# Performance work log

Hardware: AMD Instinct MI355X
Metric: run time of the kernel (lower is better)

The kernel has to match this reference:

```python
import jax, jax.numpy as jnp
import numpy as np

VOCAB, EMB, HID, LAYERS = 23, 16, 256, 8


def _lstm_layer(xseq, Wih, Whh, bih, bhh):
    # xseq: [B,T,D_in]; Wih: [4H,D_in]; Whh: [4H,H]; biases: [4H]
    B = xseq.shape[0]
    H = Whh.shape[1]
    # precompute input contribution to gates for all timesteps
    xg = jnp.einsum('btd,gd->btg', xseq, Wih) + bih + bhh  # [B,T,4H]
    xg = jnp.swapaxes(xg, 0, 1)  # [T,B,4H] for scan

    def step(carry, g_in):
        h, c = carry
        g = g_in + h @ Whh.T  # [B,4H]
        i, f, gg, o = jnp.split(g, 4, axis=-1)  # PyTorch gate order i,f,g,o
        i = jax.nn.sigmoid(i)
        f = jax.nn.sigmoid(f)
        gg = jnp.tanh(gg)
        o = jax.nn.sigmoid(o)
        c = f * c + i * gg
        h = o * jnp.tanh(c)
        return (h, c), h

    h0 = jnp.zeros((B, H), xseq.dtype)
    c0 = jnp.zeros((B, H), xseq.dtype)
    (_, _), hs = jax.lax.scan(step, (h0, c0), xg)
    return jnp.swapaxes(hs, 0, 1)  # [B,T,H]


def setup_inputs() -> dict:
    key = jax.random.key(0)
    ks = jax.random.split(key, 8)
    B, T = 64, 512
    s_e = 1.0 / np.sqrt(HID)
    x = jax.random.randint(ks[0], (B, T), 0, VOCAB)
    emb = jax.random.normal(ks[1], (VOCAB, EMB), jnp.float32)
    W_ih0 = jax.random.uniform(ks[2], (4 * HID, EMB), jnp.float32, -s_e, s_e)
    W_ih_rest = jax.random.uniform(ks[3], (LAYERS - 1, 4 * HID, HID), jnp.float32, -s_e, s_e)
    W_hh = jax.random.uniform(ks[4], (LAYERS, 4 * HID, HID), jnp.float32, -s_e, s_e)
    b_ih = jax.random.uniform(ks[5], (LAYERS, 4 * HID), jnp.float32, -s_e, s_e)
    b_hh = jax.random.uniform(ks[6], (LAYERS, 4 * HID), jnp.float32, -s_e, s_e)
    fc_w = jax.random.uniform(ks[7], (VOCAB, HID), jnp.float32, -s_e, s_e)
    fc_b = jnp.zeros((VOCAB,), jnp.float32)
    return {"x": x, "emb": emb, "W_ih0": W_ih0, "W_ih_rest": W_ih_rest,
            "W_hh": W_hh, "b_ih": b_ih, "b_hh": b_hh, "fc_w": fc_w, "fc_b": fc_b}


def reference(x, emb, W_ih0, W_ih_rest, W_hh, b_ih, b_hh, fc_w, fc_b):
    h = emb[x]  # [B,T,EMB]
    h = _lstm_layer(h, W_ih0, W_hh[0], b_ih[0], b_hh[0])
    for l in range(1, LAYERS):
        h = _lstm_layer(h, W_ih_rest[l - 1], W_hh[l], b_ih[l], b_hh[l])
    return h @ fc_w.T + fc_b  # [B,T,VOCAB]
```

## Files before the change

kernel.cpp:

```cpp
#include <hip/hip_runtime.h>
#include <cstdint>
#include <cstddef>

#define BB   64
#define TT   512
#define HH   256
#define G4   1024
#define NL   8
#define NW   32
#define HPW  8
#define NR   32

#define POLL_BOUND (1 << 15)

typedef _Float16 half8 __attribute__((ext_vector_type(8)));
typedef float   floatx4 __attribute__((ext_vector_type(4)));

__device__ __forceinline__ float sigm(float v)   { return 1.0f / (1.0f + __expf(-v)); }
__device__ __forceinline__ float tanh_f(float v) { return 1.0f - 2.0f / (__expf(2.0f * v) + 1.0f); }

__device__ __forceinline__ void gstore8_x(_Float16* p, half8 d) {
  asm volatile("global_store_dwordx4 %0, %1, off sc0 sc1" :: "v"(p), "v"(d) : "memory");
}
__device__ __forceinline__ void stdword_x(int* p, int v) {
  asm volatile("global_store_dword %0, %1, off sc0 sc1" :: "v"(p), "v"(v) : "memory");
}
__device__ __forceinline__ void wait_vm0() {
  asm volatile("s_waitcnt vmcnt(0)" ::: "memory");
}
__device__ __forceinline__ int ldflag_x(const int* p) {
  int v; asm volatile("global_load_dword %0, %1, off sc0 sc1" : "=v"(v) : "v"(p) : "memory");
  wait_vm0(); return v;
}

#define TSTRIDE ((size_t)32 * BB * 8)
#define LSTRIDE ((size_t)TT * TSTRIDE)

__global__ void build_xg0(const float* __restrict__ emb, const float* __restrict__ Wih0,
                          float* __restrict__ table) {
  int i = blockIdx.x * 256 + threadIdx.x;
  if (i >= 23 * G4) return;
  int v = i >> 10, n = i & (G4 - 1);
  float a = 0.f;
#pragma unroll
  for (int e = 0; e < 16; ++e) a += emb[v * 16 + e] * Wih0[n * 16 + e];
  table[i] = a;
}

__global__ __launch_bounds__(256, 1) void lstm_pipeline(
    const int*   __restrict__ x,
    const float* __restrict__ Wih_rest,
    const float* __restrict__ Whh,
    const float* __restrict__ bih,
    const float* __restrict__ bhh,
    const float* __restrict__ xg0t,
    _Float16* __restrict__ hseq,
    int* __restrict__ cnt)
{
  const int l   = blockIdx.x & 7;
  const int w   = blockIdx.x >> 3;
  const int tid = threadIdx.x;
  const int lane = tid & 63;
  const int p    = tid >> 6;

  __shared__ __align__(16) _Float16 wlds[64 * NR * 8];
  __shared__ __align__(16) _Float16 hl[BB * 8];
  __shared__ float  blds[NR];
  __shared__ float  tlds[23 * NR];

  for (int idx = tid; idx < 64 * NR; idx += 256) {
    int kc = idx >> 5;
    int n  = idx & 31;
    int g = n >> 3, jl = n & 7;
    int gr = g * 256 + w * HPW + jl;
    float v[8];
    if (kc < 32) {
      if (l == 0) { for (int j = 0; j < 8; ++j) v[j] = 0.f; }
      else {
        const float* src = Wih_rest + ((size_t)(l - 1) * G4 + gr) * HH + kc * 8;
        for (int j = 0; j < 8; ++j) v[j] = src[j];
      }
    } else {
      const float* src = Whh + ((size_t)l * G4 + gr) * HH + (kc - 32) * 8;
      for (int j = 0; j < 8; ++j) v[j] = src[j];
    }
    _Float16* dst = wlds + (size_t)idx * 8;
    for (int j = 0; j < 8; ++j) dst[j] = (_Float16)v[j];
  }
  if (tid < NR) {
    int g = tid >> 3, jl = tid & 7;
    int gr = g * 256 + w * HPW + jl;
    blds[tid] = bih[l * G4 + gr] + bhh[l * G4 + gr];
  }
  if (l == 0) {
    for (int idx = tid; idx < 23 * NR; idx += 256) {
      int v = idx >> 5, n = idx & 31;
      int g = n >> 3, jl = n & 7;
      tlds[idx] = xg0t[v * G4 + g * 256 + w * HPW + jl];
    }
  }
  if (tid == 0) (void)__hip_atomic_load(cnt, __ATOMIC_ACQUIRE, __HIP_MEMORY_SCOPE_AGENT);
  __syncthreads();

  const int arow = p * 16 + (lane & 15);
  const int kq   = lane >> 4;
  const int n0   = lane & 15;
  const int n1   = 16 + n0;
  const int cu   = lane & 7;
  const bool lowh = (n0 < 8);
  const int roff = lowh ? 0 : 2;
  const int rowb = p * 16 + kq * 4;

  const _Float16* hin  = hseq + (size_t)(l > 0 ? l - 1 : 0) * LSTRIDE;
  _Float16*       hrec = hseq + (size_t)l * LSTRIDE;

  const float bi = blds[cu], bf = blds[8 + cu], bg = blds[16 + cu], bo = blds[24 + cu];

  float cst[2] = {0.f, 0.f};

  for (int t = 0; t < TT; ++t) {
    floatx4 acc0 = {0.f, 0.f, 0.f, 0.f};
    floatx4 acc1 = {0.f, 0.f, 0.f, 0.f};

    if (l > 0 && t > 0) {
      const _Float16* ain = hin + (size_t)t * TSTRIDE;
      half8 aA[8];
#pragma unroll
      for (int kt = 0; kt < 8; ++kt) {
        int kc = kt * 4 + kq;
        aA[kt] = *(const half8*)(ain + ((size_t)(kc * 64 + arow) << 3));
      }
#pragma unroll
      for (int kt = 0; kt < 8; ++kt) {
        int kc = kt * 4 + kq;
        half8 w0 = *(const half8*)(wlds + ((kc * 32 + n0) << 3));
        half8 w1 = *(const half8*)(wlds + ((kc * 32 + n1) << 3));
        acc0 = __builtin_amdgcn_mfma_f32_16x16x32_f16(aA[kt], w0, acc0, 0, 0, 0);
        acc1 = __builtin_amdgcn_mfma_f32_16x16x32_f16(aA[kt], w1, acc1, 0, 0, 0);
      }
    }

    if (t > 0 && p == 3) {
      const int* f = cnt + l * NW;
      for (int it = 0; it < POLL_BOUND; ++it) {
        int v = ldflag_x(f + (lane & 31));
        if (__all(v >= t)) break;
        __builtin_amdgcn_s_sleep(1);
      }
    }
    if (l > 0 && p == 2) {
      const int tgt = (t + 2 < TT) ? t + 2 : TT;
      const int* f = cnt + (l - 1) * NW;
      for (int it = 0; it < POLL_BOUND; ++it) {
        int v = ldflag_x(f + (lane & 31));
        if (__all(v >= tgt)) break;
        __builtin_amdgcn_s_sleep(1);
      }
    }
    __syncthreads();

    if (l > 0 && t == 0) {
      const _Float16* ain = hin;
      half8 aA[8];
#pragma unroll
      for (int kt = 0; kt < 8; ++kt) {
        int kc = kt * 4 + kq;
        aA[kt] = *(const half8*)(ain + ((size_t)(kc * 64 + arow) << 3));
      }
#pragma unroll
      for (int kt = 0; kt < 8; ++kt) {
        int kc = kt * 4 + kq;
        half8 w0 = *(const half8*)(wlds + ((kc * 32 + n0) << 3));
        half8 w1 = *(const half8*)(wlds + ((kc * 32 + n1) << 3));
        acc0 = __builtin_amdgcn_mfma_f32_16x16x32_f16(aA[kt], w0, acc0, 0, 0, 0);
        acc1 = __builtin_amdgcn_mfma_f32_16x16x32_f16(aA[kt], w1, acc1, 0, 0, 0);
      }
    }

    if (t > 0) {
      const _Float16* ain = hrec + (size_t)(t - 1) * TSTRIDE;
      half8 aB[8];
#pragma unroll
      for (int kt = 0; kt < 8; ++kt) {
        int kc = kt * 4 + kq;
        aB[kt] = *(const half8*)(ain + ((size_t)(kc * 64 + arow) << 3));
      }
#pragma unroll
      for (int kt = 0; kt < 8; ++kt) {
        int kc = kt * 4 + kq;
        half8 w0 = *(const half8*)(wlds + (((32 + kc) * 32 + n0) << 3));
        half8 w1 = *(const half8*)(wlds + (((32 + kc) * 32 + n1) << 3));
        acc0 = __builtin_amdgcn_mfma_f32_16x16x32_f16(aB[kt], w0, acc0, 0, 0, 0);
        acc1 = __builtin_amdgcn_mfma_f32_16x16x32_f16(aB[kt], w1, acc1, 0, 0, 0);
      }
    }

    const float sa0 = lowh ? acc0[2] : acc0[0];
    const float sa1 = lowh ? acc0[3] : acc0[1];
    const float sb0 = lowh ? acc1[2] : acc1[0];
    const float sb1 = lowh ? acc1[3] : acc1[1];
    const float ra0 = __shfl_xor(sa0, 8);
    const float ra1 = __shfl_xor(sa1, 8);
    const float rb0 = __shfl_xor(sb0, 8);
    const float rb1 = __shfl_xor(sb1, 8);

#pragma unroll
    for (int rr = 0; rr < 2; ++rr) {
      const int r = roff + rr;
      const float own0 = acc0[r], own1 = acc1[r];
      const float oth0 = rr ? ra1 : ra0;
      const float oth1 = rr ? rb1 : rb0;
      float gi = (lowh ? own0 : oth0) + bi;
      float gf = (lowh ? oth0 : own0) + bf;
      float gg = (lowh ? own1 : oth1) + bg;
      float go = (lowh ? oth1 : own1) + bo;
      if (l == 0) {
        const int xv = x[(rowb + r) * TT + t];
        const float* tb = tlds + xv * NR;
        gi += tb[cu]; gf += tb[8 + cu]; gg += tb[16 + cu]; go += tb[24 + cu];
      }
      const float iv = sigm(gi), fv = sigm(gf), gv = tanh_f(gg), ov = sigm(go);
      cst[rr] = fv * cst[rr] + iv * gv;
      const float hv = ov * tanh_f(cst[rr]);
      hl[(rowb + r) * 8 + cu] = (_Float16)hv;
    }
    __syncthreads();

    if (tid < 64) {
      half8 hv = *(const half8*)(hl + tid * 8);
      gstore8_x(hrec + (size_t)t * TSTRIDE + ((size_t)(w * 64 + tid) << 3), hv);
      wait_vm0();
      if (tid == 0)
        stdword_x(cnt + l * NW + w, t + 1);
    }
  }
}

__global__ __launch_bounds__(256) void fc_kernel(
    const _Float16* __restrict__ hseq7,
    const float* __restrict__ fcw,
    const float* __restrict__ fcb,
    float* __restrict__ out)
{
  const int t = blockIdx.x;
  const int tid = threadIdx.x;
  __shared__ __align__(16) _Float16 hbuf[32 * 64 * 8];
  __shared__ float wbuf[23 * 256];
  __shared__ float bbuf[24];

  const _Float16* src = hseq7 + (size_t)t * TSTRIDE;
  for (int i = tid; i < 32 * 64; i += 256)
    ((half8*)hbuf)[i] = ((const half8*)src)[i];
  for (int i = tid; i < 23 * 256; i += 256) wbuf[i] = fcw[i];
  if (tid < 23) bbuf[tid] = fcb[tid];
  __syncthreads();

  for (int o = tid; o < 64 * 23; o += 256) {
    int b = o / 23, v = o - b * 23;
    float acc = bbuf[v];
#pragma unroll 4
    for (int kc = 0; kc < 32; ++kc) {
      half8 hv = *(const half8*)(hbuf + ((kc * 64 + b) << 3));
      const float* wr = wbuf + v * 256 + kc * 8;
#pragma unroll
      for (int j = 0; j < 8; ++j) acc += (float)hv[j] * wr[j];
    }
    out[((size_t)b * TT + t) * 23 + v] = acc;
  }
}

extern "C" void kernel_launch(void* const* d_in, const int* in_sizes, int n_in,
                              void* d_out, int out_size, void* d_ws, size_t ws_size,
                              hipStream_t stream) {
  const int*   x        = (const int*)d_in[0];
  const float* emb      = (const float*)d_in[1];
  const float* Wih0     = (const float*)d_in[2];
  const float* Wih_rest = (const float*)d_in[3];
  const float* Whh      = (const float*)d_in[4];
  const float* bihp     = (const float*)d_in[5];
  const float* bhhp     = (const float*)d_in[6];
  const float* fcw      = (const float*)d_in[7];
  const float* fcb      = (const float*)d_in[8];
  float* out = (float*)d_out;

  char* ws = (char*)d_ws;
  int*      cnt   = (int*)ws;
  float*    table = (float*)(ws + 16384);
  _Float16* hseq  = (_Float16*)(ws + 131072);

  hipMemsetAsync(ws, 0, 16384, stream);
  build_xg0<<<(23 * G4 + 255) / 256, 256, 0, stream>>>(emb, Wih0, table);
  lstm_pipeline<<<NL * NW, 256, 0, stream>>>(x, Wih_rest, Whh, bihp, bhhp, table, hseq, cnt);
  fc_kernel<<<TT, 256, 0, stream>>>(hseq + (size_t)7 * LSTRIDE, fcw, fcb, out);
}
```

Baseline: 1.867 ms.

## Use MFMA with split-fp16 weights in FC kernel and raise publish priority

Measured after the change: 1.602 ms. 14.2% less time.

```diff
diff --git a/kernel.cpp b/kernel.cpp
--- a/kernel.cpp
+++ b/kernel.cpp
@@ -227,11 +227,13 @@
     __syncthreads();
 
     if (tid < 64) {
+      __builtin_amdgcn_s_setprio(1);
       half8 hv = *(const half8*)(hl + tid * 8);
       gstore8_x(hrec + (size_t)t * TSTRIDE + ((size_t)(w * 64 + tid) << 3), hv);
       wait_vm0();
       if (tid == 0)
         stdword_x(cnt + l * NW + w, t + 1);
+      __builtin_amdgcn_s_setprio(0);
     }
   }
 }
@@ -244,28 +246,61 @@
 {
   const int t = blockIdx.x;
   const int tid = threadIdx.x;
-  __shared__ __align__(16) _Float16 hbuf[32 * 64 * 8];
-  __shared__ float wbuf[23 * 256];
-  __shared__ float bbuf[24];
+  const int lane = tid & 63;
+  const int p = tid >> 6;
+
+  __shared__ __align__(16) _Float16 whi[32 * 32 * 8];
+  __shared__ __align__(16) _Float16 wlo[32 * 32 * 8];
+  __shared__ float bbuf[32];
+
+  for (int idx = tid; idx < 32 * 32; idx += 256) {
+    int kc = idx >> 5, n = idx & 31;
+    _Float16* dh = whi + (size_t)idx * 8;
+    _Float16* dl = wlo + (size_t)idx * 8;
+    if (n < 23) {
+      const float* src = fcw + n * 256 + kc * 8;
+      for (int j = 0; j < 8; ++j) {
+        float v = src[j];
+        _Float16 hi = (_Float16)v;
+        dh[j] = hi;
+        dl[j] = (_Float16)((v - (float)hi) * 2048.0f);
+      }
+    } else {
+      for (int j = 0; j < 8; ++j) { dh[j] = (_Float16)0.f; dl[j] = (_Float16)0.f; }
+    }
+  }
+  if (tid < 32) bbuf[tid] = (tid < 23) ? fcb[tid] : 0.f;
+  __syncthreads();
+
+  const int arow = p * 16 + (lane & 15);
+  const int kq   = lane >> 4;
+  const int n0   = lane & 15;
+  const int n1   = 16 + n0;
 
   const _Float16* src = hseq7 + (size_t)t * TSTRIDE;
-  for (int i = tid; i < 32 * 64; i += 256)
-    ((half8*)hbuf)[i] = ((const half8*)src)[i];
-  for (int i = tid; i < 23 * 256; i += 256) wbuf[i] = fcw[i];
-  if (tid < 23) bbuf[tid] = fcb[tid];
-  __syncthreads();
-
-  for (int o = tid; o < 64 * 23; o += 256) {
-    int b = o / 23, v = o - b * 23;
-    float acc = bbuf[v];
-#pragma unroll 4
-    for (int kc = 0; kc < 32; ++kc) {
-      half8 hv = *(const half8*)(hbuf + ((kc * 64 + b) << 3));
-      const float* wr = wbuf + v * 256 + kc * 8;
-#pragma unroll
-      for (int j = 0; j < 8; ++j) acc += (float)hv[j] * wr[j];
-    }
-    out[((size_t)b * TT + t) * 23 + v] = acc;
+  floatx4 a0h = {0.f,0.f,0.f,0.f}, a1h = {0.f,0.f,0.f,0.f};
+  floatx4 a0l = {0.f,0.f,0.f,0.f}, a1l = {0.f,0.f,0.f,0.f};
+#pragma unroll
+  for (int kt = 0; kt < 8; ++kt) {
+    int kc = kt * 4 + kq;
+    half8 a  = *(const half8*)(src + ((size_t)(kc * 64 + arow) << 3));
+    half8 h0 = *(const half8*)(whi + ((kc * 32 + n0) << 3));
+    half8 h1 = *(const half8*)(whi + ((kc * 32 + n1) << 3));
+    half8 l0 = *(const half8*)(wlo + ((kc * 32 + n0) << 3));
+    half8 l1 = *(const half8*)(wlo + ((kc * 32 + n1) << 3));
+    a0h = __builtin_amdgcn_mfma_f32_16x16x32_f16(a, h0, a0h, 0, 0, 0);
+    a1h = __builtin_amdgcn_mfma_f32_16x16x32_f16(a, h1, a1h, 0, 0, 0);
+    a0l = __builtin_amdgcn_mfma_f32_16x16x32_f16(a, l0, a0l, 0, 0, 0);
+    a1l = __builtin_amdgcn_mfma_f32_16x16x32_f16(a, l1, a1l, 0, 0, 0);
+  }
+
+  const float rs = 1.0f / 2048.0f;
+#pragma unroll
+  for (int r = 0; r < 4; ++r) {
+    int b = p * 16 + kq * 4 + r;
+    out[((size_t)b * TT + t) * 23 + n0] = a0h[r] + a0l[r] * rs + bbuf[n0];
+    if (n1 < 23)
+      out[((size_t)b * TT + t) * 23 + n1] = a1h[r] + a1l[r] * rs + bbuf[n1];
   }
 }
 
```
